# Kernel tuning notes

Hardware: AMD Instinct MI355X
Metric: run time of the kernel (lower is better)

## Reference

```python
import jax, jax.numpy as jnp
import numpy as np

DISTANCES = [1, 2]
ANGLES_DEG = [0.0, 45.0, 90.0, 135.0]
LEVELS = 32
FEATURES = ["contrast", "homogeneity", "energy", "correlation"]

# skimage graycomatrix offsets: row = r + round(sin(a)*d), col = c + round(cos(a)*d)
OFFSETS = [(int(np.round(np.sin(np.deg2rad(a)) * d)), int(np.round(np.cos(np.deg2rad(a)) * d)))
           for d in DISTANCES for a in ANGLES_DEG]


def _quantize(images, levels):
    # RGB -> gray, [-1,1] -> [0,1] -> integer gray levels (uint8 floor cast in original)
    gray = images.mean(axis=1)                                  # [B,H,W]
    g = jnp.clip((gray + 1.0) * 0.5 * (levels - 1), 0.0, levels - 1)
    return g.astype(jnp.int32)


def _glcm(g, dr, dc, levels):
    # symmetric, normed co-occurrence matrix for one (distance, angle) offset
    B, H, W = g.shape
    r0, r1 = max(0, -dr), H - max(0, dr)
    c0, c1 = max(0, -dc), W - max(0, dc)
    i = g[:, r0:r1, c0:c1]
    j = g[:, r0 + dr:r1 + dr, c0 + dc:c1 + dc]
    idx = (i * levels + j).reshape(B, -1)                        # [B, n_pairs]
    hist = jax.vmap(lambda ix: jnp.zeros(levels * levels, jnp.float32).at[ix].add(1.0))(idx)
    P = hist.reshape(B, levels, levels)
    P = P + jnp.swapaxes(P, 1, 2)                                # symmetric
    return P / jnp.sum(P, axis=(1, 2), keepdims=True)            # normed


def _prop(P, feat):
    # graycoprops formulas; P: [B, L, L]
    L = P.shape[-1]
    I = jnp.arange(L, dtype=jnp.float32)[:, None]                # [L,1]
    J = jnp.arange(L, dtype=jnp.float32)[None, :]                # [1,L]
    if feat == "contrast":
        return jnp.sum(P * (I - J) ** 2, axis=(1, 2))
    if feat == "homogeneity":
        return jnp.sum(P / (1.0 + (I - J) ** 2), axis=(1, 2))
    if feat == "energy":
        return jnp.sqrt(jnp.sum(P * P, axis=(1, 2)))
    if feat == "correlation":
        mu_i = jnp.sum(I * P, axis=(1, 2))                       # [B]
        mu_j = jnp.sum(J * P, axis=(1, 2))
        di = I[None] - mu_i[:, None, None]
        dj = J[None] - mu_j[:, None, None]
        std_i = jnp.sqrt(jnp.sum(P * di * di, axis=(1, 2)))
        std_j = jnp.sqrt(jnp.sum(P * dj * dj, axis=(1, 2)))
        cov = jnp.sum(P * di * dj, axis=(1, 2))
        denom = std_i * std_j
        return jnp.where(denom > 1e-15, cov / jnp.where(denom > 1e-15, denom, 1.0), 1.0)
    raise ValueError(feat)


def reference(images):
    g = _quantize(images, LEVELS)
    # accumulate feature values over all (distance, angle) offsets, then mean
    acc = {f: 0.0 for f in FEATURES}
    for (dr, dc) in OFFSETS:
        P = _glcm(g, dr, dc, LEVELS)
        for f in FEATURES:
            acc[f] = acc[f] + _prop(P, f)
    n = float(len(OFFSETS))
    return jnp.stack([acc[f] / n for f in FEATURES], axis=0)     # [n_features, B]


def setup_inputs() -> dict:
    key = jax.random.key(0)
    images = jax.random.normal(key, (64, 3, 512, 512), dtype=jnp.float32)
    return {"images": images}
```

## Files before the change

kernel.cpp:

```cpp
#include <hip/hip_runtime.h>

typedef unsigned int uint;

#define HW (512 * 512)
#define NIMG 64
#define NUQ 6
#define NBAND 8

__device__ __constant__ float UOFF_W[NUQ] = {1.f, 2.f, 1.f, 2.f, 1.f, 1.f};
__device__ __constant__ float NPAIRS[NUQ] = {
    512.f * 511.f, 511.f * 511.f, 511.f * 512.f,
    511.f * 511.f, 512.f * 510.f, 510.f * 512.f};

__device__ __forceinline__ uint q1f(float a, float b, float c) {
    float t = fmaf(a + b + c, 5.1666665f, 15.5f);
    t = fminf(fmaxf(t, 0.0f), 31.0f);
    return (uint)t;
}

__global__ __launch_bounds__(256) void glcm_fused(
    const float* __restrict__ in, uint* __restrict__ wire) {
    __shared__ __align__(16) uint hist[8192];
    const int tid = threadIdx.x;
    const int b = blockIdx.x >> 3;
    const int band = blockIdx.x & 7;
    const int cg = tid & 31;
    const int ts = tid >> 5;
    const int r0 = band * 64 + ts * 8;
    const int c0 = cg << 4;
    const float* ib = in + (size_t)b * (3 * HW);
    unsigned char* hb8 = (unsigned char*)hist;

    {
        uint4 z = make_uint4(0, 0, 0, 0);
        #pragma unroll
        for (int q = 0; q < 8; ++q)
            *(uint4*)(hb8 + tid * 16 + q * 4096) = z;
    }
    __syncthreads();

    auto qrow = [&](int r, uint w[5]) {
        const float* base = ib + ((size_t)r << 9);
        #pragma unroll
        for (int k = 0; k < 5; ++k) {
            int cc = (k < 4) ? (c0 + 4 * k) : min(c0 + 16, 508);
            float4 f0 = *(const float4*)(base + cc);
            float4 f1 = *(const float4*)(base + HW + cc);
            float4 f2 = *(const float4*)(base + 2 * HW + cc);
            w[k] = (q1f(f0.x, f1.x, f2.x) << 2)
                 | (q1f(f0.y, f1.y, f2.y) << 10)
                 | (q1f(f0.z, f1.z, f2.z) << 18)
                 | (q1f(f0.w, f1.w, f2.w) << 26);
        }
        if (cg == 31) w[4] = 0x80808080u;
    };

    auto pp = [&](uint IW, uint JW, int tagoff, uint inc) {
        uint a0 = __builtin_amdgcn_perm(IW, JW, 0x0C0C0400u) & 0xFCFCu;
        uint a1 = __builtin_amdgcn_perm(IW, JW, 0x0C0C0501u) & 0xFCFCu;
        uint a2 = __builtin_amdgcn_perm(IW, JW, 0x0C0C0602u) & 0xFCFCu;
        uint a3 = __builtin_amdgcn_perm(IW, JW, 0x0C0C0703u) & 0xFCFCu;
        atomicAdd((uint*)(hb8 + tagoff + a0), inc);
        atomicAdd((uint*)(hb8 + tagoff + a1), inc);
        atomicAdd((uint*)(hb8 + tagoff + a2), inc);
        atomicAdd((uint*)(hb8 + tagoff + a3), inc);
    };

    uint p2[5] = {0, 0, 0, 0, 0}, p1[5] = {0, 0, 0, 0, 0}, cur[5];
    if (r0 >= 2) qrow(r0 - 2, p2);
    if (r0 >= 1) qrow(r0 - 1, p1);

    for (int it = 0; it < 8; ++it) {
        const int r = r0 + it;
        qrow(r, cur);

        #pragma unroll
        for (int k = 0; k < 4; ++k) {
            uint C1 = __builtin_amdgcn_alignbyte(cur[k + 1], cur[k], 1);
            uint C2 = __builtin_amdgcn_alignbyte(cur[k + 1], cur[k], 2);
            pp(cur[k], C1, 0,   1u);
            pp(cur[k], C2, 256, 65536u);
        }
        if (r >= 1) {
            #pragma unroll
            for (int k = 0; k < 4; ++k) {
                uint C1 = __builtin_amdgcn_alignbyte(cur[k + 1], cur[k], 1);
                uint P1 = __builtin_amdgcn_alignbyte(p1[k + 1], p1[k], 1);
                pp(p1[k], cur[k], 512, 1u);
                pp(p1[k], C1,     256, 1u);
                pp(cur[k], P1,    0,   65536u);
            }
            if (r >= 2) {
                #pragma unroll
                for (int k = 0; k < 4; ++k)
                    pp(p2[k], cur[k], 512, 65536u);
            }
        }
        #pragma unroll
        for (int k = 0; k < 5; ++k) { p2[k] = p1[k]; p1[k] = cur[k]; }
    }
    __syncthreads();

    uint* hw = wire + (size_t)blockIdx.x * 3072;
    #pragma unroll
    for (int qq = 0; qq < 12; ++qq) {
        int o = tid + qq * 256;
        int tg = o >> 10, ij = o & 1023;
        int i = ij >> 5, j = ij & 31;
        hw[o] = hist[(i << 8) | (tg << 6) | j];
    }
}

__global__ __launch_bounds__(256) void feature_out_kernel(
    const uint* __restrict__ wire, float* __restrict__ out) {
    const int b = blockIdx.x;
    __shared__ uint cnt[NUQ][1024];
    __shared__ float fred[NUQ][4];
    const int tid = threadIdx.x, wid = tid >> 6, lane = tid & 63;

    for (int u = wid; u < NUQ; u += 4) {
        const int tg = (u < 3) ? u : u - 3;
        const int sh = (u < 3) ? 0 : 16;
        const uint* p = wire + (size_t)b * (NBAND * 3072) + tg * 1024;
        for (int ij = lane; ij < 1024; ij += 64) {
            uint acc = 0;
            #pragma unroll
            for (int st = 0; st < NBAND; ++st)
                acc += (p[(size_t)st * 3072 + ij] >> sh) & 0xFFFFu;
            cnt[u][ij] = acc;
        }
    }
    __syncthreads();

    for (int u = wid; u < NUQ; u += 4) {
        const float inv_total = 1.0f / (2.0f * NPAIRS[u]);
        float c_sum = 0, h_sum = 0, e_sum = 0, m1 = 0, m2 = 0, m12 = 0;
        for (int k = lane; k < 1024; k += 64) {
            int i = k >> 5, j = k & 31;
            float sym = (float)(cnt[u][k] + cnt[u][(j << 5) | i]);
            float P = sym * inv_total;
            float d = (float)(i - j);
            float d2 = d * d;
            float fi = (float)i, fj = (float)j;
            c_sum += P * d2;
            h_sum += P / (1.0f + d2);
            e_sum += P * P;
            m1 += P * fi; m2 += P * fi * fi; m12 += P * fi * fj;
        }
        #pragma unroll
        for (int sft = 32; sft > 0; sft >>= 1) {
            c_sum += __shfl_down(c_sum, sft);
            h_sum += __shfl_down(h_sum, sft);
            e_sum += __shfl_down(e_sum, sft);
            m1 += __shfl_down(m1, sft);
            m2 += __shfl_down(m2, sft);
            m12 += __shfl_down(m12, sft);
        }
        if (lane == 0) {
            float mu = m1, var = m2 - mu * mu, cov = m12 - mu * mu;
            float corr = (var > 1e-15f) ? cov / var : 1.0f;
            fred[u][0] = c_sum; fred[u][1] = h_sum;
            fred[u][2] = sqrtf(e_sum); fred[u][3] = corr;
        }
    }
    __syncthreads();
    if (tid < 4) {
        float acc = 0.f;
        #pragma unroll
        for (int u = 0; u < NUQ; ++u) acc += UOFF_W[u] * fred[u][tid];
        out[tid * NIMG + b] = acc * 0.125f;
    }
}

extern "C" void kernel_launch(void* const* d_in, const int* in_sizes, int n_in,
                              void* d_out, int out_size, void* d_ws, size_t ws_size,
                              hipStream_t stream) {
    const float* images = (const float*)d_in[0];
    float* out = (float*)d_out;
    uint* wire = (uint*)d_ws;

    glcm_fused<<<NIMG * NBAND, 256, 0, stream>>>(images, wire);
    feature_out_kernel<<<NIMG, 256, 0, stream>>>(wire, out);
}
```

Measured before the change: 81.46 us.

## Stage quantized rows in LDS ring buffers and skew histogram bins

Each block now handles two 32-row strips. It quantizes rows into two shared-memory ring buffers while histogramming the other strip, so global loads overlap with LDS atomics. Each row is loaded once by coalesced threads instead of being reloaded with halo columns per thread. The histogram column index is skewed by 3*i to spread LDS bank conflicts among the atomics, and the writeout undoes the skew. This costs more shared memory per block, which may lower occupancy, and adds barriers in every pipeline step.

```diff
diff --git a/kernel.cpp b/kernel.cpp
--- a/kernel.cpp
+++ b/kernel.cpp
@@ -5,7 +5,12 @@
 #define HW (512 * 512)
 #define NIMG 64
 #define NUQ 6
-#define NBAND 8
+#define RSTRIDE 528
+#define RINGROWS 16
+#define RINGBYTES (RINGROWS * RSTRIDE)
+#define RINGA 32768
+#define RINGB (32768 + RINGBYTES)
+#define SMEMB (32768 + 2 * RINGBYTES)
 
 __device__ __constant__ float UOFF_W[NUQ] = {1.f, 2.f, 1.f, 2.f, 1.f, 1.f};
 __device__ __constant__ float NPAIRS[NUQ] = {
@@ -20,94 +25,117 @@
 
 __global__ __launch_bounds__(256) void glcm_fused(
     const float* __restrict__ in, uint* __restrict__ wire) {
-    __shared__ __align__(16) uint hist[8192];
+    __shared__ __align__(16) unsigned char smem[SMEMB];
     const int tid = threadIdx.x;
     const int b = blockIdx.x >> 3;
-    const int band = blockIdx.x & 7;
-    const int cg = tid & 31;
-    const int ts = tid >> 5;
-    const int r0 = band * 64 + ts * 8;
-    const int c0 = cg << 4;
+    const int sp = blockIdx.x & 7;
+    const int rsA = sp * 32;
+    const int rsB = sp * 32 + 256;
     const float* ib = in + (size_t)b * (3 * HW);
-    unsigned char* hb8 = (unsigned char*)hist;
+    const int lrow = tid >> 6;
+    const int lcol = (tid & 63) << 3;
 
     {
         uint4 z = make_uint4(0, 0, 0, 0);
         #pragma unroll
         for (int q = 0; q < 8; ++q)
-            *(uint4*)(hb8 + tid * 16 + q * 4096) = z;
+            *(uint4*)(smem + tid * 16 + q * 4096) = z;
     }
     __syncthreads();
 
-    auto qrow = [&](int r, uint w[5]) {
-        const float* base = ib + ((size_t)r << 9);
-        #pragma unroll
-        for (int k = 0; k < 5; ++k) {
-            int cc = (k < 4) ? (c0 + 4 * k) : min(c0 + 16, 508);
-            float4 f0 = *(const float4*)(base + cc);
-            float4 f1 = *(const float4*)(base + HW + cc);
-            float4 f2 = *(const float4*)(base + 2 * HW + cc);
-            w[k] = (q1f(f0.x, f1.x, f2.x) << 2)
-                 | (q1f(f0.y, f1.y, f2.y) << 10)
-                 | (q1f(f0.z, f1.z, f2.z) << 18)
-                 | (q1f(f0.w, f1.w, f2.w) << 26);
-        }
-        if (cg == 31) w[4] = 0x80808080u;
+    auto issueL = [&](int rs, int c, float4& A0, float4& B0, float4& A1,
+                      float4& B1, float4& A2, float4& B2) {
+        int R = rs - 2 + 4 * c + lrow;
+        int Rc = min(max(R, 0), 511);
+        const float* p = ib + ((size_t)Rc << 9) + lcol;
+        A0 = *(const float4*)(p);
+        B0 = *(const float4*)(p + 4);
+        A1 = *(const float4*)(p + HW);
+        B1 = *(const float4*)(p + HW + 4);
+        A2 = *(const float4*)(p + 2 * HW);
+        B2 = *(const float4*)(p + 2 * HW + 4);
     };
 
-    auto pp = [&](uint IW, uint JW, int tagoff, uint inc) {
-        uint a0 = __builtin_amdgcn_perm(IW, JW, 0x0C0C0400u) & 0xFCFCu;
-        uint a1 = __builtin_amdgcn_perm(IW, JW, 0x0C0C0501u) & 0xFCFCu;
-        uint a2 = __builtin_amdgcn_perm(IW, JW, 0x0C0C0602u) & 0xFCFCu;
-        uint a3 = __builtin_amdgcn_perm(IW, JW, 0x0C0C0703u) & 0xFCFCu;
-        atomicAdd((uint*)(hb8 + tagoff + a0), inc);
-        atomicAdd((uint*)(hb8 + tagoff + a1), inc);
-        atomicAdd((uint*)(hb8 + tagoff + a2), inc);
-        atomicAdd((uint*)(hb8 + tagoff + a3), inc);
+    auto quantW = [&](int rs, int ringo, int c, const float4& A0, const float4& B0,
+                      const float4& A1, const float4& B1, const float4& A2,
+                      const float4& B2) {
+        int R = rs - 2 + 4 * c + lrow;
+        if (R >= 0 && R <= 511) {
+            uint q0 = (q1f(A0.x, A1.x, A2.x) << 2)
+                    | (q1f(A0.y, A1.y, A2.y) << 10)
+                    | (q1f(A0.z, A1.z, A2.z) << 18)
+                    | (q1f(A0.w, A1.w, A2.w) << 26);
+            uint q1_ = (q1f(B0.x, B1.x, B2.x) << 2)
+                     | (q1f(B0.y, B1.y, B2.y) << 10)
+                     | (q1f(B0.z, B1.z, B2.z) << 18)
+                     | (q1f(B0.w, B1.w, B2.w) << 26);
+            unsigned char* rw = smem + ringo + ((R + 2) & 15) * RSTRIDE;
+            *(uint2*)(rw + lcol) = make_uint2(q0, q1_);
+            if ((tid & 63) == 63)
+                *(uint4*)(rw + 512) = make_uint4(0x80808080u, 0x80808080u,
+                                                 0x80808080u, 0x80808080u);
+        }
     };
 
-    uint p2[5] = {0, 0, 0, 0, 0}, p1[5] = {0, 0, 0, 0, 0}, cur[5];
-    if (r0 >= 2) qrow(r0 - 2, p2);
-    if (r0 >= 1) qrow(r0 - 1, p1);
-
-    for (int it = 0; it < 8; ++it) {
-        const int r = r0 + it;
-        qrow(r, cur);
-
-        #pragma unroll
-        for (int k = 0; k < 4; ++k) {
-            uint C1 = __builtin_amdgcn_alignbyte(cur[k + 1], cur[k], 1);
-            uint C2 = __builtin_amdgcn_alignbyte(cur[k + 1], cur[k], 2);
-            pp(cur[k], C1, 0,   1u);
-            pp(cur[k], C2, 256, 65536u);
-        }
-        if (r >= 1) {
-            #pragma unroll
-            for (int k = 0; k < 4; ++k) {
-                uint C1 = __builtin_amdgcn_alignbyte(cur[k + 1], cur[k], 1);
-                uint P1 = __builtin_amdgcn_alignbyte(p1[k + 1], p1[k], 1);
-                pp(p1[k], cur[k], 512, 1u);
-                pp(p1[k], C1,     256, 1u);
-                pp(cur[k], P1,    0,   65536u);
-            }
-            if (r >= 2) {
-                #pragma unroll
-                for (int k = 0; k < 4; ++k)
-                    pp(p2[k], cur[k], 512, 65536u);
-            }
-        }
-        #pragma unroll
-        for (int k = 0; k < 5; ++k) { p2[k] = p1[k]; p1[k] = cur[k]; }
-    }
-    __syncthreads();
+    auto histC = [&](int rs, int ringo, int h) {
+        const unsigned char* ring = smem + ringo;
+        #pragma unroll
+        for (int rr = 0; rr < 2; ++rr) {
+            const int R = rs + 4 * h + 2 * rr + (tid >> 7);
+            const int dq = tid & 127;
+            const uint* rowL   = (const uint*)(ring + ((R + 2) & 15) * RSTRIDE);
+            const uint* rowLm  = (const uint*)(ring + ((R + 1) & 15) * RSTRIDE);
+            const uint* rowLp  = (const uint*)(ring + ((R + 3) & 15) * RSTRIDE);
+            const uint* rowLpp = (const uint*)(ring + ((R + 4) & 15) * RSTRIDE);
+            uint A  = rowL[dq],  A1 = rowL[dq + 1];
+            uint Bm = rowLp[dq], B1 = rowLp[dq + 1];
+            uint Cm = rowLm[dq], C1 = rowLm[dq + 1];
+            uint D  = rowLpp[dq];
+
+            auto pp4 = [&](uint IW, uint JW, int tagoff, uint inc) {
+                uint jm = (JW >> 2) & 0x1F1F1F1Fu;
+                uint im = (IW >> 2) & 0x1F1F1F1Fu;
+                uint s  = (jm + im + (im << 1)) & 0x1F1F1F1Fu;
+                uint J2 = (s << 2) | (JW & 0x80808080u);
+                uint a0 = __builtin_amdgcn_perm(IW, J2, 0x0C0C0400u);
+                uint a1 = __builtin_amdgcn_perm(IW, J2, 0x0C0C0501u);
+                uint a2 = __builtin_amdgcn_perm(IW, J2, 0x0C0C0602u);
+                uint a3 = __builtin_amdgcn_perm(IW, J2, 0x0C0C0703u);
+                atomicAdd((uint*)(smem + tagoff + a0), inc);
+                atomicAdd((uint*)(smem + tagoff + a1), inc);
+                atomicAdd((uint*)(smem + tagoff + a2), inc);
+                atomicAdd((uint*)(smem + tagoff + a3), inc);
+            };
+            if (R < 512) pp4(A, __builtin_amdgcn_alignbyte(A1, A, 1), 0, 1u);
+            if (R < 511) pp4(A, __builtin_amdgcn_alignbyte(B1, Bm, 1), 256, 1u);
+            if (R < 511) pp4(A, Bm, 512, 1u);
+            if (R >= 1 && R < 512)
+                pp4(A, __builtin_amdgcn_alignbyte(C1, Cm, 1), 0, 65536u);
+            if (R < 512) pp4(A, __builtin_amdgcn_alignbyte(A1, A, 2), 256, 65536u);
+            if (R < 510) pp4(A, D, 512, 65536u);
+        }
+    };
+
+    float4 a0, b0, a1, b1, a2, b2;
+    for (int i = 0; i < 10; ++i) {
+        if (i <= 8) issueL(rsA, i, a0, b0, a1, b1, a2, b2);
+        if (i >= 2) histC(rsB, RINGB, i - 2);
+        if (i <= 8) quantW(rsA, RINGA, i, a0, b0, a1, b1, a2, b2);
+        __syncthreads();
+        if (i <= 8) issueL(rsB, i, a0, b0, a1, b1, a2, b2);
+        if (i >= 2) histC(rsA, RINGA, i - 2);
+        if (i <= 8) quantW(rsB, RINGB, i, a0, b0, a1, b1, a2, b2);
+        __syncthreads();
+    }
 
     uint* hw = wire + (size_t)blockIdx.x * 3072;
+    const uint* hist = (const uint*)smem;
     #pragma unroll
     for (int qq = 0; qq < 12; ++qq) {
         int o = tid + qq * 256;
         int tg = o >> 10, ij = o & 1023;
-        int i = ij >> 5, j = ij & 31;
-        hw[o] = hist[(i << 8) | (tg << 6) | j];
+        int i2 = ij >> 5, j = ij & 31;
+        hw[o] = hist[(i2 << 8) | (tg << 6) | ((j + 3 * i2) & 31)];
     }
 }
 
@@ -121,11 +149,11 @@
     for (int u = wid; u < NUQ; u += 4) {
         const int tg = (u < 3) ? u : u - 3;
         const int sh = (u < 3) ? 0 : 16;
-        const uint* p = wire + (size_t)b * (NBAND * 3072) + tg * 1024;
+        const uint* p = wire + (size_t)b * (8 * 3072) + tg * 1024;
         for (int ij = lane; ij < 1024; ij += 64) {
             uint acc = 0;
             #pragma unroll
-            for (int st = 0; st < NBAND; ++st)
+            for (int st = 0; st < 8; ++st)
                 acc += (p[(size_t)st * 3072 + ij] >> sh) & 0xFFFFu;
             cnt[u][ij] = acc;
         }
@@ -179,6 +207,6 @@
     float* out = (float*)d_out;
     uint* wire = (uint*)d_ws;
 
-    glcm_fused<<<NIMG * NBAND, 256, 0, stream>>>(images, wire);
+    glcm_fused<<<NIMG * 8, 256, 0, stream>>>(images, wire);
     feature_out_kernel<<<NIMG, 256, 0, stream>>>(wire, out);
 }
```

After: 74.04 us. 9.1% less time.
